# Performance work log

Hardware: AMD Instinct MI355X
Metric: run time of the kernel (lower is better)

The kernel has to match this reference:

```python
import jax, jax.numpy as jnp
import numpy as np

# ---- static configuration (matches init_kwargs / input_specs) ----
B, DIM, H, W = 2, 32, 512, 512
FOLD, P, HDIM, NCLS, CV = 8, 2, 96, 16, 96
S = P * P                      # superpixels per tile
h, w = H // FOLD, W // FOLD    # 64, 64 tile size
N = h * w                      # pixels per tile

# ---- static SSN neighbor tables (init label map -> 9 candidate spixels) ----
_lab = np.repeat(np.repeat(np.arange(S).reshape(P, P), h // P, 0), w // P, 1).reshape(-1)
_sy, _sx = _lab // P, _lab % P
_dy = np.repeat(np.array([-1, 0, 1]), 3)[:, None]
_dx = np.tile(np.array([-1, 0, 1]), 3)[:, None]
_ny, _nx = _sy[None] + _dy, _sx[None] + _dx
_valid = (_ny >= 0) & (_ny < P) & (_nx >= 0) & (_nx < P)
NBR = jnp.asarray(np.where(_valid, _ny * P + _nx, 0), dtype=jnp.int32)  # [9,N]
VALID = jnp.asarray(_valid)                                             # [9,N]

def _conv1x1(x, Wk, bk):
    return jnp.einsum('oc,bchw->bohw', Wk, x) + bk[None, :, None, None]

def _tiles(t):  # 'b c (f1 h) (f2 w) -> (b f1 f2) c h w'
    Bq, C = t.shape[:2]
    return t.reshape(Bq, C, FOLD, h, FOLD, w).transpose(0, 2, 4, 1, 3, 5).reshape(Bq * FOLD * FOLD, C, h, w)

def _pool(t):  # adaptive avg pool (h,w)->(P,P); returns [b,C,S]
    b, C = t.shape[:2]
    return t.reshape(b, C, P, h // P, P, w // P).mean((3, 5)).reshape(b, C, S)

def _affinity(Fp, cen):
    # Fp [b,Ctot,N], cen [b,Ctot,S]; squared-euclid dist pixel->9 neighbor spixels,
    # sparse softmax over the 9 candidates, then scatter to dense [b,S,N] affinity.
    d = (Fp * Fp).sum(1)[:, None, :] + (cen * cen).sum(1)[:, :, None] \
        - 2.0 * jnp.einsum('bcn,bcs->bsn', Fp, cen)          # [b,S,N]
    b = Fp.shape[0]
    idx = jnp.broadcast_to(NBR[None], (b, 9, N))
    d9 = jnp.where(VALID[None], jnp.take_along_axis(d, idx, axis=1), 1e16)
    aff = jax.nn.softmax(-d9, axis=1)                        # [b,9,N]
    bi = jnp.arange(b)[:, None, None]
    ni = jnp.arange(N)[None, None, :]
    return jnp.zeros((b, S, N), Fp.dtype).at[bi, idx, ni].add(jnp.where(VALID[None], aff, 0.0))

def setup_inputs():
    k = jax.random.split(jax.random.key(0), 6)
    return {
        'x': jax.random.normal(k[0], (B, DIM, H, W), jnp.float32),
        'feat': jax.random.normal(k[1], (B, CV, H, W), jnp.float32),
        'sdf_data': jax.random.normal(k[2], (B, DIM - 1, H, W), jnp.float32),
        'Wf': 0.1 * jax.random.normal(k[3], (HDIM, DIM), jnp.float32),
        'bf': jnp.zeros((HDIM,), jnp.float32),
        'Wsdf': 0.1 * jax.random.normal(k[4], (HDIM, DIM - 1), jnp.float32),
        'bsdf': jnp.zeros((HDIM,), jnp.float32),
        'gt': jax.random.randint(k[5], (B, H, W), 0, NCLS, jnp.int32),
    }

def _cluster(x, feat, sdf_data, Wf, bf, Wsdf, bsdf):
    hsi = _conv1x1(x, Wf, bf)
    sdf = _conv1x1(sdf_data, Wsdf, bsdf)
    pf = _tiles(feat).reshape(-1, CV, N)      # per-tile pixel (value) features
    df = _tiles(hsi).reshape(-1, HDIM, N)     # deep features
    sf = _tiles(sdf).reshape(-1, HDIM, N)     # sdf features
    b = pf.shape[0]
    cen_pf = _pool(pf.reshape(b, CV, h, w))
    cen_df = _pool(df.reshape(b, HDIM, h, w))
    cen_sf = _pool(sf.reshape(b, HDIM, h, w))
    value_centers = cen_pf.transpose(0, 2, 1)                # [b,S,C]
    Fall = jnp.concatenate([pf, df, sf], 1)
    # SSN iter 0: soft affinity, update pixel-feature centroids
    A0 = _affinity(Fall, jnp.concatenate([cen_pf, cen_df, cen_sf], 1))
    cen_pf = jnp.einsum('bsn,bcn->bcs', A0, pf) / (A0.sum(-1)[:, None, :] + 1e-16)
    # SSN iter 1 (last): final dense affinity; torch computes this under no_grad
    sim = jax.lax.stop_gradient(_affinity(Fall, jnp.concatenate([cen_pf, cen_df, cen_sf], 1)))
    mask = jax.nn.one_hot(jnp.argmax(sim, 1), S, axis=1, dtype=sim.dtype)   # hard argmax mask [b,S,N]
    sim = sim * mask
    out = (jnp.einsum('bsn,bnc->bsc', sim, pf.transpose(0, 2, 1)) + value_centers) \
          / (sim.sum(-1, keepdims=True) + 1.0)
    center_feat = out.reshape(B, FOLD * FOLD * S, CV)
    mask5 = mask.reshape(B, FOLD * FOLD, S, h, w)
    return center_feat, mask5

def _gen_labels(gt, mask5):
    T = FOLD * FOLD
    coef = jnp.arange(S, dtype=mask5.dtype).reshape(1, 1, S, 1, 1)
    small = (mask5 * coef).sum(2) + jnp.arange(0, T * S, S, dtype=mask5.dtype).reshape(1, T, 1, 1)
    spix_map = small.reshape(B, FOLD, FOLD, h, w).transpose(0, 1, 3, 2, 4).reshape(B, H, W)
    gt_r = gt.reshape(B, FOLD, h, FOLD, w).transpose(0, 1, 3, 2, 4).reshape(B, T, h, w) + 1
    gt_filt = (gt_r[:, :, None].astype(mask5.dtype) * mask5).reshape(B, T, S, N).astype(jnp.int32)
    count = jax.nn.one_hot(gt_filt, NCLS + 1, dtype=jnp.float32).sum(3)   # [B,T,S,NCLS+1]
    labels = count[..., 1:].transpose(0, 3, 1, 2).reshape(B, NCLS, T * S)
    return labels, spix_map

def reference(x, feat, sdf_data, Wf, bf, Wsdf, bsdf, gt):
    center_feat, mask5 = _cluster(x, feat, sdf_data, Wf, bf, Wsdf, bsdf)
    labels, spix_map = _gen_labels(gt, jax.lax.stop_gradient(mask5))
    return center_feat, labels, spix_map
```

## Files before the change

kernel.cpp:

```cpp
#include <hip/hip_runtime.h>
#include <hip/hip_bf16.h>


#define OFF_POOLX   0
#define OFF_POOLS   16384
#define OFF_CENPF0  32256
#define OFF_UDF     81408
#define OFF_USF     97792
#define OFF_GCONST  113664
#define OFF_NORM0   114176
#define OFF_NUM1    114688
#define OFF_DEN1    163840
#define OFF_CENPF1  164352
#define OFF_NORM1   213504
#define OFF_OUTNUM  214016
#define OFF_OUTDEN  263168
#define OFF_LABELS  263680
#define OFF_G       271872

#define OUT_CF 0
#define OUT_LB 49152
#define OUT_SP 57344

typedef float f32x4 __attribute__((ext_vector_type(4)));
typedef short bf16x8 __attribute__((ext_vector_type(8)));

__device__ __forceinline__ float bf2f(unsigned short u) {
  return __uint_as_float(((unsigned)u) << 16);
}
__device__ __forceinline__ unsigned short f2bf(float f) {
  return (unsigned short)(__float_as_uint(f) >> 16);
}

__global__ __launch_bounds__(256) void k_pool(const float* __restrict__ x,
    const float* __restrict__ feat, const float* __restrict__ sdf,
    float* __restrict__ ws) {
  int plane = blockIdx.x, f1 = blockIdx.y, tid = threadIdx.x;
  int b = plane / 159, ch = plane % 159;
  const float* src; int c, C, cls;
  if (ch < 32)      { src = x;    C = 32; c = ch;      cls = 0; }
  else if (ch < 63) { src = sdf;  C = 31; c = ch - 32; cls = 1; }
  else              { src = feat; C = 96; c = ch - 63; cls = 2; }
  const float* base = src + ((size_t)(b*C + c)*512 + f1*64)*512;
  int half = tid >> 7, col4 = tid & 127;
  const float* p0 = base + (size_t)half*512 + (size_t)col4*4;
  float4 v[16];
  float acc0 = 0.f, acc1 = 0.f;
  #pragma unroll
  for (int i = 0; i < 16; ++i)
    v[i] = *reinterpret_cast<const float4*>(p0 + (size_t)i*1024);
  #pragma unroll
  for (int i = 0; i < 16; ++i) { float4 t = v[i]; acc0 += t.x + t.y + t.z + t.w; }
  #pragma unroll
  for (int i = 0; i < 16; ++i)
    v[i] = *reinterpret_cast<const float4*>(p0 + (size_t)(16 + i)*1024);
  #pragma unroll
  for (int i = 0; i < 16; ++i) { float4 t = v[i]; acc1 += t.x + t.y + t.z + t.w; }
  acc0 += __shfl_xor(acc0, 1, 64); acc0 += __shfl_xor(acc0, 2, 64); acc0 += __shfl_xor(acc0, 4, 64);
  acc1 += __shfl_xor(acc1, 1, 64); acc1 += __shfl_xor(acc1, 2, 64); acc1 += __shfl_xor(acc1, 4, 64);
  __shared__ float part[32][2];
  int lane = tid & 63;
  if ((lane & 7) == 0) {
    int f2 = col4 >> 4, qx = (col4 >> 3) & 1;
    part[(f2*2 + qx)*2 + 0][half] = acc0;
    part[(f2*2 + qx)*2 + 1][half] = acc1;
  }
  __syncthreads();
  if (tid < 32) {
    float v2 = (part[tid][0] + part[tid][1]) * (1.f/1024.f);
    int f2 = tid >> 2, qx = (tid >> 1) & 1, qy = tid & 1;
    int tile = b*64 + f1*8 + f2, s = qy*2 + qx;
    float* dst;
    if (cls == 0)      dst = ws + OFF_POOLX  + (tile*32 + c)*4;
    else if (cls == 1) dst = ws + OFF_POOLS  + (tile*31 + c)*4;
    else               dst = ws + OFF_CENPF0 + (tile*96 + c)*4;
    dst[s] = v2;
  }
}

__global__ __launch_bounds__(384) void k_centers(const float* __restrict__ Wf,
    const float* __restrict__ bfv, const float* __restrict__ Wsdf,
    const float* __restrict__ bsdf, float* __restrict__ ws) {
  int tile = blockIdx.x, tid = threadIdx.x;
  __shared__ float px[128];
  __shared__ float ps[124];
  __shared__ float cdf[384];
  __shared__ float csf[384];
  __shared__ float redg[4], redn[4];
  if (tid < 128) px[tid] = ws[OFF_POOLX + tile*128 + tid];
  if (tid < 124) ps[tid] = ws[OFF_POOLS + tile*124 + tid];
  if (tid < 4) { redg[tid] = 0.f; redn[tid] = 0.f; }
  __syncthreads();
  int c = tid % 96, s = tid / 96;
  float bc = bfv[c];
  float a = bc;
  for (int k = 0; k < 32; ++k) a += Wf[c*32 + k] * px[k*4 + s];
  cdf[c*4 + s] = a;
  float bs = bsdf[c];
  float a2 = bs;
  for (int k = 0; k < 31; ++k) a2 += Wsdf[c*31 + k] * ps[k*4 + s];
  csf[c*4 + s] = a2;
  atomicAdd(&redg[s], 2.f*(bc*a + bs*a2) - (a*a + a2*a2));
  float cp = ws[OFF_CENPF0 + tile*384 + c*4 + s];
  atomicAdd(&redn[s], cp*cp);
  __syncthreads();
  if (tid < 128) {
    int s2 = tid >> 5, k = tid & 31;
    float u = 0.f;
    for (int c2 = 0; c2 < 96; ++c2) u += Wf[c2*32 + k] * cdf[c2*4 + s2];
    ws[OFF_UDF + tile*128 + tid] = u;
  } else if (tid < 252) {
    int t2 = tid - 128, s2 = t2 / 31, k = t2 % 31;
    float u = 0.f;
    for (int c2 = 0; c2 < 96; ++c2) u += Wsdf[c2*31 + k] * csf[c2*4 + s2];
    ws[OFF_USF + tile*124 + t2] = u;
  }
  if (tid < 4) { ws[OFF_GCONST + tile*4 + tid] = redg[tid]; ws[OFF_NORM0 + tile*4 + tid] = redn[tid]; }
}

__global__ __launch_bounds__(256) void k_pass2(const float* __restrict__ x,
    const float* __restrict__ feat, const float* __restrict__ sdf,
    float* __restrict__ ws) {
  int wg = blockIdx.x, tile = wg >> 2, seg = wg & 3, tid = threadIdx.x;
  int b = tile >> 6, tl = tile & 63, f1 = tl >> 3, f2 = tl & 7;
  __shared__ float s_cpf0[384];
  __shared__ float s_udf[128];
  __shared__ float s_usf[124];
  __shared__ float s_gc[4], s_n0[4];
  __shared__ __align__(16) unsigned short s_pfT[96][264];
  __shared__ __align__(16) unsigned short s_aT[16][264];
  for (int i = tid; i < 384; i += 256) s_cpf0[i] = ws[OFF_CENPF0 + tile*384 + i];
  if (tid < 128) s_udf[tid] = ws[OFF_UDF + tile*128 + tid];
  if (tid < 124) s_usf[tid] = ws[OFF_USF + tile*124 + tid];
  if (tid < 4) { s_gc[tid] = ws[OFF_GCONST + tile*4 + tid]; s_n0[tid] = ws[OFF_NORM0 + tile*4 + tid]; }
  for (int i = tid; i < 16*264; i += 256) (&s_aT[0][0])[i] = 0;
  __syncthreads();
  int lane = tid & 63, wave = tid >> 6;
  int mrow = lane & 15, quad = lane >> 4;
  f32x4 zero4 = {0.f, 0.f, 0.f, 0.f};
  f32x4 accC[6] = {zero4, zero4, zero4, zero4, zero4, zero4};
  float dden[4] = {0.f, 0.f, 0.f, 0.f};
  for (int chunk = 0; chunk < 4; ++chunk) {
    int p = seg*1024 + chunk*256 + tid;
    int y = p >> 6, xx = p & 63;
    int go = (f1*64 + y)*512 + f2*64 + xx;
    const float* xp = x   + (size_t)b*32*262144 + go;
    const float* sp = sdf + (size_t)b*31*262144 + go;
    const float* fp = feat+ (size_t)b*96*262144 + go;
    float vv[16];
    float d0=0.f,d1=0.f,d2=0.f,d3=0.f;
    #pragma unroll
    for (int kb = 0; kb < 32; kb += 16) {
      #pragma unroll
      for (int j = 0; j < 16; ++j) vv[j] = xp[(size_t)(kb + j)*262144];
      #pragma unroll
      for (int j = 0; j < 16; ++j) {
        float v = vv[j]; int k = kb + j;
        d0 += v*s_udf[k]; d1 += v*s_udf[32+k]; d2 += v*s_udf[64+k]; d3 += v*s_udf[96+k];
      }
    }
    {
      #pragma unroll
      for (int j = 0; j < 16; ++j) vv[j] = sp[(size_t)j*262144];
      #pragma unroll
      for (int j = 0; j < 16; ++j) {
        float v = vv[j];
        d0 += v*s_usf[j]; d1 += v*s_usf[31+j]; d2 += v*s_usf[62+j]; d3 += v*s_usf[93+j];
      }
      #pragma unroll
      for (int j = 0; j < 15; ++j) vv[j] = sp[(size_t)(16 + j)*262144];
      #pragma unroll
      for (int j = 0; j < 15; ++j) {
        float v = vv[j]; int k = 16 + j;
        d0 += v*s_usf[k]; d1 += v*s_usf[31+k]; d2 += v*s_usf[62+k]; d3 += v*s_usf[93+k];
      }
    }
    float g0 = 2.f*d0 + s_gc[0], g1 = 2.f*d1 + s_gc[1];
    float g2 = 2.f*d2 + s_gc[2], g3 = 2.f*d3 + s_gc[3];
    int gbase = OFF_G + (tile << 14) + p;
    ws[gbase] = g0; ws[gbase + 4096] = g1; ws[gbase + 8192] = g2; ws[gbase + 12288] = g3;
    float p0=0.f,p1=0.f,p2=0.f,p3=0.f;
    #pragma unroll
    for (int cb = 0; cb < 96; cb += 16) {
      #pragma unroll
      for (int j = 0; j < 16; ++j) vv[j] = fp[(size_t)(cb + j)*262144];
      #pragma unroll
      for (int j = 0; j < 16; ++j) {
        float v = vv[j]; int cc = cb + j;
        s_pfT[cc][tid] = f2bf(v);
        p0 += v*s_cpf0[cc*4+0]; p1 += v*s_cpf0[cc*4+1]; p2 += v*s_cpf0[cc*4+2]; p3 += v*s_cpf0[cc*4+3];
      }
    }
    float sc0 = g0 + 2.f*p0 - s_n0[0];
    float sc1 = g1 + 2.f*p1 - s_n0[1];
    float sc2 = g2 + 2.f*p2 - s_n0[2];
    float sc3 = g3 + 2.f*p3 - s_n0[3];
    float m = fmaxf(fmaxf(sc0, sc1), fmaxf(sc2, sc3));
    float e0 = expf(sc0 - m), e1 = expf(sc1 - m), e2 = expf(sc2 - m), e3 = expf(sc3 - m);
    float inv = 1.f / (e0 + e1 + e2 + e3);
    float a0 = e0*inv, a1 = e1*inv, a2 = e2*inv, a3 = e3*inv;
    s_aT[0][tid] = f2bf(a0); s_aT[1][tid] = f2bf(a1);
    s_aT[2][tid] = f2bf(a2); s_aT[3][tid] = f2bf(a3);
    dden[0] += a0; dden[1] += a1; dden[2] += a2; dden[3] += a3;
    __syncthreads();
    #pragma unroll
    for (int kk = 0; kk < 2; ++kk) {
      int k0 = (wave*2 + kk)*32 + quad*8;
      bf16x8 bfrag = *reinterpret_cast<const bf16x8*>(&s_aT[mrow][k0]);
      #pragma unroll
      for (int mt = 0; mt < 6; ++mt) {
        bf16x8 afrag = *reinterpret_cast<const bf16x8*>(&s_pfT[mt*16 + mrow][k0]);
        accC[mt] = __builtin_amdgcn_mfma_f32_16x16x32_bf16(afrag, bfrag, accC[mt], 0, 0, 0);
      }
    }
    __syncthreads();
  }
  if (mrow < 4) {
    #pragma unroll
    for (int mt = 0; mt < 6; ++mt)
      #pragma unroll
      for (int r = 0; r < 4; ++r) {
        int c = mt*16 + quad*4 + r;
        atomicAdd(&ws[OFF_NUM1 + (tile*96 + c)*4 + mrow], accC[mt][r]);
      }
  }
  for (int m2 = 1; m2 < 64; m2 <<= 1) {
    dden[0] += __shfl_xor(dden[0], m2, 64); dden[1] += __shfl_xor(dden[1], m2, 64);
    dden[2] += __shfl_xor(dden[2], m2, 64); dden[3] += __shfl_xor(dden[3], m2, 64);
  }
  if (lane == 0) {
    atomicAdd(&ws[OFF_DEN1 + tile*4 + 0], dden[0]);
    atomicAdd(&ws[OFF_DEN1 + tile*4 + 1], dden[1]);
    atomicAdd(&ws[OFF_DEN1 + tile*4 + 2], dden[2]);
    atomicAdd(&ws[OFF_DEN1 + tile*4 + 3], dden[3]);
  }
}

__global__ __launch_bounds__(384) void k_fin1(float* __restrict__ ws) {
  int tile = blockIdx.x, tid = threadIdx.x;
  __shared__ float red[4];
  if (tid < 4) red[tid] = 0.f;
  __syncthreads();
  int c = tid % 96, s = tid / 96;
  float den = ws[OFF_DEN1 + tile*4 + s];
  float v = ws[OFF_NUM1 + (tile*96 + c)*4 + s] / (den + 1e-16f);
  ws[OFF_CENPF1 + (tile*96 + c)*4 + s] = v;
  atomicAdd(&red[s], v*v);
  __syncthreads();
  if (tid < 4) ws[OFF_NORM1 + tile*4 + tid] = red[tid];
}

__global__ __launch_bounds__(256) void k_pass3(const float* __restrict__ feat,
    const int* __restrict__ gt, float* __restrict__ ws, float* __restrict__ out) {
  int wg = blockIdx.x, tile = wg >> 2, seg = wg & 3, tid = threadIdx.x;
  int b = tile >> 6, tl = tile & 63, f1 = tl >> 3, f2 = tl & 7;
  __shared__ float s_cpf1[384];
  __shared__ float s_n1[4];
  __shared__ __align__(16) unsigned short s_pfT[96][264];
  __shared__ __align__(16) unsigned short s_aT[16][264];
  __shared__ float s_hist[64];
  for (int i = tid; i < 384; i += 256) s_cpf1[i] = ws[OFF_CENPF1 + tile*384 + i];
  if (tid < 4) s_n1[tid] = ws[OFF_NORM1 + tile*4 + tid];
  if (tid < 64) s_hist[tid] = 0.f;
  for (int i = tid; i < 16*264; i += 256) (&s_aT[0][0])[i] = 0;
  __syncthreads();
  int lane = tid & 63, wave = tid >> 6;
  int mrow = lane & 15, quad = lane >> 4;
  f32x4 zero4 = {0.f, 0.f, 0.f, 0.f};
  f32x4 accC[6] = {zero4, zero4, zero4, zero4, zero4, zero4};
  float oden[4] = {0.f, 0.f, 0.f, 0.f};
  for (int chunk = 0; chunk < 4; ++chunk) {
    int p = seg*1024 + chunk*256 + tid;
    int y = p >> 6, xx = p & 63;
    int go = (f1*64 + y)*512 + f2*64 + xx;
    int gbase = OFF_G + (tile << 14) + p;
    float g0 = ws[gbase], g1 = ws[gbase + 4096], g2 = ws[gbase + 8192], g3 = ws[gbase + 12288];
    const float* fp = feat + (size_t)b*96*262144 + go;
    float vv[16];
    float p0=0.f,p1=0.f,p2=0.f,p3=0.f;
    #pragma unroll
    for (int cb = 0; cb < 96; cb += 16) {
      #pragma unroll
      for (int j = 0; j < 16; ++j) vv[j] = fp[(size_t)(cb + j)*262144];
      #pragma unroll
      for (int j = 0; j < 16; ++j) {
        float v = vv[j]; int cc = cb + j;
        s_pfT[cc][tid] = f2bf(v);
        p0 += v*s_cpf1[cc*4+0]; p1 += v*s_cpf1[cc*4+1]; p2 += v*s_cpf1[cc*4+2]; p3 += v*s_cpf1[cc*4+3];
      }
    }
    float sc0 = g0 + 2.f*p0 - s_n1[0];
    float sc1 = g1 + 2.f*p1 - s_n1[1];
    float sc2 = g2 + 2.f*p2 - s_n1[2];
    float sc3 = g3 + 2.f*p3 - s_n1[3];
    int ss = 0; float best = sc0;
    if (sc1 > best) { best = sc1; ss = 1; }
    if (sc2 > best) { best = sc2; ss = 2; }
    if (sc3 > best) { best = sc3; ss = 3; }
    float se = expf(sc0-best) + expf(sc1-best) + expf(sc2-best) + expf(sc3-best);
    float sim = 1.f / se;
    unsigned short sb = f2bf(sim);
    s_aT[0][tid] = (ss == 0) ? sb : (unsigned short)0;
    s_aT[1][tid] = (ss == 1) ? sb : (unsigned short)0;
    s_aT[2][tid] = (ss == 2) ? sb : (unsigned short)0;
    s_aT[3][tid] = (ss == 3) ? sb : (unsigned short)0;
    oden[ss] += sim;
    int gv = gt[b*262144 + go];
    atomicAdd(&s_hist[ss*16 + gv], 1.f);
    out[OUT_SP + b*262144 + go] = (float)(tl*4 + ss);
    __syncthreads();
    #pragma unroll
    for (int kk = 0; kk < 2; ++kk) {
      int k0 = (wave*2 + kk)*32 + quad*8;
      bf16x8 bfrag = *reinterpret_cast<const bf16x8*>(&s_aT[mrow][k0]);
      #pragma unroll
      for (int mt = 0; mt < 6; ++mt) {
        bf16x8 afrag = *reinterpret_cast<const bf16x8*>(&s_pfT[mt*16 + mrow][k0]);
        accC[mt] = __builtin_amdgcn_mfma_f32_16x16x32_bf16(afrag, bfrag, accC[mt], 0, 0, 0);
      }
    }
    __syncthreads();
  }
  if (mrow < 4) {
    #pragma unroll
    for (int mt = 0; mt < 6; ++mt)
      #pragma unroll
      for (int r = 0; r < 4; ++r) {
        int c = mt*16 + quad*4 + r;
        atomicAdd(&ws[OFF_OUTNUM + (tile*96 + c)*4 + mrow], accC[mt][r]);
      }
  }
  for (int m2 = 1; m2 < 64; m2 <<= 1) {
    oden[0] += __shfl_xor(oden[0], m2, 64); oden[1] += __shfl_xor(oden[1], m2, 64);
    oden[2] += __shfl_xor(oden[2], m2, 64); oden[3] += __shfl_xor(oden[3], m2, 64);
  }
  if (lane == 0) {
    atomicAdd(&ws[OFF_OUTDEN + tile*4 + 0], oden[0]);
    atomicAdd(&ws[OFF_OUTDEN + tile*4 + 1], oden[1]);
    atomicAdd(&ws[OFF_OUTDEN + tile*4 + 2], oden[2]);
    atomicAdd(&ws[OFF_OUTDEN + tile*4 + 3], oden[3]);
  }
  if (tid < 64) atomicAdd(&ws[OFF_LABELS + tile*64 + tid], s_hist[tid]);
}

__global__ __launch_bounds__(384) void k_out(const float* __restrict__ ws,
                                             float* __restrict__ out) {
  int tile = blockIdx.x, tid = threadIdx.x;
  int b = tile >> 6, tl = tile & 63;
  int c = tid % 96, s = tid / 96;
  float od = ws[OFF_OUTDEN + tile*4 + s];
  float v = (ws[OFF_OUTNUM + (tile*96 + c)*4 + s] + ws[OFF_CENPF0 + (tile*96 + c)*4 + s]) / (od + 1.f);
  out[OUT_CF + (size_t)(b*256 + tl*4 + s)*96 + c] = v;
  if (tid < 64) {
    int s2 = tid >> 4, cls = tid & 15;
    float cnt = ws[OFF_LABELS + tile*64 + tid];
    out[OUT_LB + (b*16 + cls)*256 + tl*4 + s2] = cnt;
  }
}

extern "C" void kernel_launch(void* const* d_in, const int* in_sizes, int n_in,
                              void* d_out, int out_size, void* d_ws, size_t ws_size,
                              hipStream_t stream) {
  const float* x    = (const float*)d_in[0];
  const float* feat = (const float*)d_in[1];
  const float* sdf  = (const float*)d_in[2];
  const float* Wf   = (const float*)d_in[3];
  const float* bfv  = (const float*)d_in[4];
  const float* Wsdf = (const float*)d_in[5];
  const float* bsdf = (const float*)d_in[6];
  const int* gt = (const int*)d_in[7];
  float* ws = (float*)d_ws;
  float* out = (float*)d_out;

  hipMemsetAsync(ws + OFF_NUM1, 0,
                 (size_t)(OFF_LABELS + 128*64 - OFF_NUM1) * sizeof(float), stream);

  k_pool   <<<dim3(318, 8), 256, 0, stream>>>(x, feat, sdf, ws);
  k_centers<<<128, 384, 0, stream>>>(Wf, bfv, Wsdf, bsdf, ws);
  k_pass2  <<<512, 256, 0, stream>>>(x, feat, sdf, ws);
  k_fin1   <<<128, 384, 0, stream>>>(ws);
  k_pass3  <<<512, 256, 0, stream>>>(feat, gt, ws, out);
  k_out    <<<128, 384, 0, stream>>>(ws, out);
}
```

Measured before the change: 507.8 us.

## Stash pooled inputs in tile-contiguous layout during pooling pass for later passes

The pooling kernel now also writes every input value it reads into a workspace stash arranged per tile, per 256-pixel group and per channel. The later passes then read from this stash instead of doing strided gathers over the NCHW inputs. The intermediate G values are also stored interleaved as one float4 per pixel, so each is a single vector store and load. This turns the later passes' reads into contiguous per-channel rows, at the cost of an extra full write and re-read of about 159 channels of data through the workspace.

```diff
diff --git a/kernel.cpp b/kernel.cpp
--- a/kernel.cpp
+++ b/kernel.cpp
@@ -17,6 +17,9 @@
 #define OFF_OUTDEN  263168
 #define OFF_LABELS  263680
 #define OFF_G       271872
+#define OFF_STASH   16777216
+#define CHSTRIDE    256
+#define GSTRIDE     40704
 
 #define OUT_CF 0
 #define OUT_LB 49152
@@ -41,40 +44,51 @@
   if (ch < 32)      { src = x;    C = 32; c = ch;      cls = 0; }
   else if (ch < 63) { src = sdf;  C = 31; c = ch - 32; cls = 1; }
   else              { src = feat; C = 96; c = ch - 63; cls = 2; }
-  const float* base = src + ((size_t)(b*C + c)*512 + f1*64)*512;
-  int half = tid >> 7, col4 = tid & 127;
-  const float* p0 = base + (size_t)half*512 + (size_t)col4*4;
+  int wave = tid >> 6, L = tid & 63;
+  const float* base = src + ((size_t)(b*C + c)*512 + f1*64 + wave*16)*512 + L*4;
+  int tile0 = b*64 + f1*8;
+  int stash0 = OFF_STASH + ch*CHSTRIDE + (L & 15)*4;
+  float accE = 0.f, accO = 0.f;
   float4 v[16];
-  float acc0 = 0.f, acc1 = 0.f;
   #pragma unroll
-  for (int i = 0; i < 16; ++i)
-    v[i] = *reinterpret_cast<const float4*>(p0 + (size_t)i*1024);
-  #pragma unroll
-  for (int i = 0; i < 16; ++i) { float4 t = v[i]; acc0 += t.x + t.y + t.z + t.w; }
-  #pragma unroll
-  for (int i = 0; i < 16; ++i)
-    v[i] = *reinterpret_cast<const float4*>(p0 + (size_t)(16 + i)*1024);
-  #pragma unroll
-  for (int i = 0; i < 16; ++i) { float4 t = v[i]; acc1 += t.x + t.y + t.z + t.w; }
-  acc0 += __shfl_xor(acc0, 1, 64); acc0 += __shfl_xor(acc0, 2, 64); acc0 += __shfl_xor(acc0, 4, 64);
-  acc1 += __shfl_xor(acc1, 1, 64); acc1 += __shfl_xor(acc1, 2, 64); acc1 += __shfl_xor(acc1, 4, 64);
-  __shared__ float part[32][2];
-  int lane = tid & 63;
-  if ((lane & 7) == 0) {
-    int f2 = col4 >> 4, qx = (col4 >> 3) & 1;
-    part[(f2*2 + qx)*2 + 0][half] = acc0;
-    part[(f2*2 + qx)*2 + 1][half] = acc1;
+  for (int jb = 0; jb < 2; ++jb) {
+    #pragma unroll
+    for (int j = 0; j < 16; ++j)
+      v[j] = *reinterpret_cast<const float4*>(base + (size_t)(jb*16 + j)*256);
+    #pragma unroll
+    for (int j = 0; j < 16; ++j) {
+      int jj = jb*16 + j;
+      int row = wave*16 + (jj >> 1);
+      int colHalf = jj & 1;
+      int f2 = colHalf*4 + (L >> 4);
+      int g = row >> 2;
+      int px = (row & 3)*64;
+      float4 t = v[j];
+      *reinterpret_cast<float4*>(ws + stash0 +
+          (size_t)((tile0 + f2)*16 + g)*GSTRIDE + px) = t;
+      float s4 = t.x + t.y + t.z + t.w;
+      if (colHalf == 0) accE += s4; else accO += s4;
+    }
+  }
+  accE += __shfl_xor(accE, 1, 64); accE += __shfl_xor(accE, 2, 64); accE += __shfl_xor(accE, 4, 64);
+  accO += __shfl_xor(accO, 1, 64); accO += __shfl_xor(accO, 2, 64); accO += __shfl_xor(accO, 4, 64);
+  __shared__ float part[4][16];
+  if ((L & 7) == 0) {
+    int qx = (L >> 3) & 1, fE = L >> 4;
+    part[wave][fE*2 + qx] = accE;
+    part[wave][(4 + fE)*2 + qx] = accO;
   }
   __syncthreads();
   if (tid < 32) {
-    float v2 = (part[tid][0] + part[tid][1]) * (1.f/1024.f);
     int f2 = tid >> 2, qx = (tid >> 1) & 1, qy = tid & 1;
-    int tile = b*64 + f1*8 + f2, s = qy*2 + qx;
+    int idx = f2*2 + qx;
+    float val = (part[qy*2][idx] + part[qy*2 + 1][idx]) * (1.f/1024.f);
+    int tile = tile0 + f2, s = qy*2 + qx;
     float* dst;
     if (cls == 0)      dst = ws + OFF_POOLX  + (tile*32 + c)*4;
     else if (cls == 1) dst = ws + OFF_POOLS  + (tile*31 + c)*4;
     else               dst = ws + OFF_CENPF0 + (tile*96 + c)*4;
-    dst[s] = v2;
+    dst[s] = val;
   }
 }
 
@@ -122,7 +136,6 @@
     const float* __restrict__ feat, const float* __restrict__ sdf,
     float* __restrict__ ws) {
   int wg = blockIdx.x, tile = wg >> 2, seg = wg & 3, tid = threadIdx.x;
-  int b = tile >> 6, tl = tile & 63, f1 = tl >> 3, f2 = tl & 7;
   __shared__ float s_cpf0[384];
   __shared__ float s_udf[128];
   __shared__ float s_usf[124];
@@ -141,18 +154,15 @@
   f32x4 accC[6] = {zero4, zero4, zero4, zero4, zero4, zero4};
   float dden[4] = {0.f, 0.f, 0.f, 0.f};
   for (int chunk = 0; chunk < 4; ++chunk) {
+    int g = seg*4 + chunk;
     int p = seg*1024 + chunk*256 + tid;
-    int y = p >> 6, xx = p & 63;
-    int go = (f1*64 + y)*512 + f2*64 + xx;
-    const float* xp = x   + (size_t)b*32*262144 + go;
-    const float* sp = sdf + (size_t)b*31*262144 + go;
-    const float* fp = feat+ (size_t)b*96*262144 + go;
+    const float* SB = ws + OFF_STASH + (size_t)(tile*16 + g)*GSTRIDE + tid;
     float vv[16];
     float d0=0.f,d1=0.f,d2=0.f,d3=0.f;
     #pragma unroll
     for (int kb = 0; kb < 32; kb += 16) {
       #pragma unroll
-      for (int j = 0; j < 16; ++j) vv[j] = xp[(size_t)(kb + j)*262144];
+      for (int j = 0; j < 16; ++j) vv[j] = SB[(size_t)(kb + j)*CHSTRIDE];
       #pragma unroll
       for (int j = 0; j < 16; ++j) {
         float v = vv[j]; int k = kb + j;
@@ -161,14 +171,14 @@
     }
     {
       #pragma unroll
-      for (int j = 0; j < 16; ++j) vv[j] = sp[(size_t)j*262144];
+      for (int j = 0; j < 16; ++j) vv[j] = SB[(size_t)(32 + j)*CHSTRIDE];
       #pragma unroll
       for (int j = 0; j < 16; ++j) {
         float v = vv[j];
         d0 += v*s_usf[j]; d1 += v*s_usf[31+j]; d2 += v*s_usf[62+j]; d3 += v*s_usf[93+j];
       }
       #pragma unroll
-      for (int j = 0; j < 15; ++j) vv[j] = sp[(size_t)(16 + j)*262144];
+      for (int j = 0; j < 15; ++j) vv[j] = SB[(size_t)(48 + j)*CHSTRIDE];
       #pragma unroll
       for (int j = 0; j < 15; ++j) {
         float v = vv[j]; int k = 16 + j;
@@ -177,13 +187,15 @@
     }
     float g0 = 2.f*d0 + s_gc[0], g1 = 2.f*d1 + s_gc[1];
     float g2 = 2.f*d2 + s_gc[2], g3 = 2.f*d3 + s_gc[3];
-    int gbase = OFF_G + (tile << 14) + p;
-    ws[gbase] = g0; ws[gbase + 4096] = g1; ws[gbase + 8192] = g2; ws[gbase + 12288] = g3;
+    {
+      f32x4 gv = {g0, g1, g2, g3};
+      *reinterpret_cast<f32x4*>(ws + OFF_G + ((size_t)tile << 14) + (size_t)p*4) = gv;
+    }
     float p0=0.f,p1=0.f,p2=0.f,p3=0.f;
     #pragma unroll
     for (int cb = 0; cb < 96; cb += 16) {
       #pragma unroll
-      for (int j = 0; j < 16; ++j) vv[j] = fp[(size_t)(cb + j)*262144];
+      for (int j = 0; j < 16; ++j) vv[j] = SB[(size_t)(63 + cb + j)*CHSTRIDE];
       #pragma unroll
       for (int j = 0; j < 16; ++j) {
         float v = vv[j]; int cc = cb + j;
@@ -270,18 +282,18 @@
   f32x4 accC[6] = {zero4, zero4, zero4, zero4, zero4, zero4};
   float oden[4] = {0.f, 0.f, 0.f, 0.f};
   for (int chunk = 0; chunk < 4; ++chunk) {
+    int g = seg*4 + chunk;
     int p = seg*1024 + chunk*256 + tid;
     int y = p >> 6, xx = p & 63;
     int go = (f1*64 + y)*512 + f2*64 + xx;
-    int gbase = OFF_G + (tile << 14) + p;
-    float g0 = ws[gbase], g1 = ws[gbase + 4096], g2 = ws[gbase + 8192], g3 = ws[gbase + 12288];
-    const float* fp = feat + (size_t)b*96*262144 + go;
+    f32x4 gv = *reinterpret_cast<const f32x4*>(ws + OFF_G + ((size_t)tile << 14) + (size_t)p*4);
+    const float* SB = ws + OFF_STASH + (size_t)(tile*16 + g)*GSTRIDE + tid;
     float vv[16];
     float p0=0.f,p1=0.f,p2=0.f,p3=0.f;
     #pragma unroll
     for (int cb = 0; cb < 96; cb += 16) {
       #pragma unroll
-      for (int j = 0; j < 16; ++j) vv[j] = fp[(size_t)(cb + j)*262144];
+      for (int j = 0; j < 16; ++j) vv[j] = SB[(size_t)(63 + cb + j)*CHSTRIDE];
       #pragma unroll
       for (int j = 0; j < 16; ++j) {
         float v = vv[j]; int cc = cb + j;
@@ -289,10 +301,10 @@
         p0 += v*s_cpf1[cc*4+0]; p1 += v*s_cpf1[cc*4+1]; p2 += v*s_cpf1[cc*4+2]; p3 += v*s_cpf1[cc*4+3];
       }
     }
-    float sc0 = g0 + 2.f*p0 - s_n1[0];
-    float sc1 = g1 + 2.f*p1 - s_n1[1];
-    float sc2 = g2 + 2.f*p2 - s_n1[2];
-    float sc3 = g3 + 2.f*p3 - s_n1[3];
+    float sc0 = gv[0] + 2.f*p0 - s_n1[0];
+    float sc1 = gv[1] + 2.f*p1 - s_n1[1];
+    float sc2 = gv[2] + 2.f*p2 - s_n1[2];
+    float sc3 = gv[3] + 2.f*p3 - s_n1[3];
     int ss = 0; float best = sc0;
     if (sc1 > best) { best = sc1; ss = 1; }
     if (sc2 > best) { best = sc2; ss = 2; }
@@ -305,8 +317,8 @@
     s_aT[2][tid] = (ss == 2) ? sb : (unsigned short)0;
     s_aT[3][tid] = (ss == 3) ? sb : (unsigned short)0;
     oden[ss] += sim;
-    int gv = gt[b*262144 + go];
-    atomicAdd(&s_hist[ss*16 + gv], 1.f);
+    int gv2 = gt[b*262144 + go];
+    atomicAdd(&s_hist[ss*16 + gv2], 1.f);
     out[OUT_SP + b*262144 + go] = (float)(tl*4 + ss);
     __syncthreads();
     #pragma unroll
```

New measurement: 561.6 us. +10.6%, slower.

## Vectorize pass loads across waves, fold memset and fin1 into other kernels

Applied to the files above, without the earlier changes.

In pass2 and pass3, each thread now loads float4 over four adjacent pixels, and the channel reduction is split across waves. Partial sums are combined through shared memory, which adds two barriers per chunk. The G buffer layout becomes pixel-interleaved so it can be written and read as one float4. The workspace memset is folded into k_pool, and the k_fin1 normalization is folded into the pass3 prologue, removing two launches.

```diff
diff --git a/kernel.cpp b/kernel.cpp
--- a/kernel.cpp
+++ b/kernel.cpp
@@ -17,6 +17,8 @@
 #define OFF_OUTDEN  263168
 #define OFF_LABELS  263680
 #define OFF_G       271872
+#define ZERO_BASE   OFF_NUM1
+#define ZERO_LEN    157184
 
 #define OUT_CF 0
 #define OUT_LB 49152
@@ -24,6 +26,7 @@
 
 typedef float f32x4 __attribute__((ext_vector_type(4)));
 typedef short bf16x8 __attribute__((ext_vector_type(8)));
+typedef unsigned short u16x4 __attribute__((ext_vector_type(4)));
 
 __device__ __forceinline__ float bf2f(unsigned short u) {
   return __uint_as_float(((unsigned)u) << 16);
@@ -36,6 +39,13 @@
     const float* __restrict__ feat, const float* __restrict__ sdf,
     float* __restrict__ ws) {
   int plane = blockIdx.x, f1 = blockIdx.y, tid = threadIdx.x;
+  {
+    int lb = blockIdx.y * gridDim.x + blockIdx.x;
+    if (tid < 64) {
+      int zi = lb * 64 + tid;
+      if (zi < ZERO_LEN) ws[ZERO_BASE + zi] = 0.f;
+    }
+  }
   int b = plane / 159, ch = plane % 159;
   const float* src; int c, C, cls;
   if (ch < 32)      { src = x;    C = 32; c = ch;      cls = 0; }
@@ -44,18 +54,18 @@
   const float* base = src + ((size_t)(b*C + c)*512 + f1*64)*512;
   int half = tid >> 7, col4 = tid & 127;
   const float* p0 = base + (size_t)half*512 + (size_t)col4*4;
-  float4 v[16];
+  f32x4 v[16];
   float acc0 = 0.f, acc1 = 0.f;
   #pragma unroll
   for (int i = 0; i < 16; ++i)
-    v[i] = *reinterpret_cast<const float4*>(p0 + (size_t)i*1024);
+    v[i] = *reinterpret_cast<const f32x4*>(p0 + (size_t)i*1024);
   #pragma unroll
-  for (int i = 0; i < 16; ++i) { float4 t = v[i]; acc0 += t.x + t.y + t.z + t.w; }
+  for (int i = 0; i < 16; ++i) { f32x4 t = v[i]; acc0 += t[0] + t[1] + t[2] + t[3]; }
   #pragma unroll
   for (int i = 0; i < 16; ++i)
-    v[i] = *reinterpret_cast<const float4*>(p0 + (size_t)(16 + i)*1024);
+    v[i] = *reinterpret_cast<const f32x4*>(p0 + (size_t)(16 + i)*1024);
   #pragma unroll
-  for (int i = 0; i < 16; ++i) { float4 t = v[i]; acc1 += t.x + t.y + t.z + t.w; }
+  for (int i = 0; i < 16; ++i) { f32x4 t = v[i]; acc1 += t[0] + t[1] + t[2] + t[3]; }
   acc0 += __shfl_xor(acc0, 1, 64); acc0 += __shfl_xor(acc0, 2, 64); acc0 += __shfl_xor(acc0, 4, 64);
   acc1 += __shfl_xor(acc1, 1, 64); acc1 += __shfl_xor(acc1, 2, 64); acc1 += __shfl_xor(acc1, 4, 64);
   __shared__ float part[32][2];
@@ -129,6 +139,7 @@
   __shared__ float s_gc[4], s_n0[4];
   __shared__ __align__(16) unsigned short s_pfT[96][264];
   __shared__ __align__(16) unsigned short s_aT[16][264];
+  __shared__ __align__(16) float s_part[2][8][260];
   for (int i = tid; i < 384; i += 256) s_cpf0[i] = ws[OFF_CENPF0 + tile*384 + i];
   if (tid < 128) s_udf[tid] = ws[OFF_UDF + tile*128 + tid];
   if (tid < 124) s_usf[tid] = ws[OFF_USF + tile*124 + tid];
@@ -137,59 +148,88 @@
   __syncthreads();
   int lane = tid & 63, wave = tid >> 6;
   int mrow = lane & 15, quad = lane >> 4;
+  int q4 = lane * 4;
   f32x4 zero4 = {0.f, 0.f, 0.f, 0.f};
   f32x4 accC[6] = {zero4, zero4, zero4, zero4, zero4, zero4};
   float dden[4] = {0.f, 0.f, 0.f, 0.f};
   for (int chunk = 0; chunk < 4; ++chunk) {
-    int p = seg*1024 + chunk*256 + tid;
-    int y = p >> 6, xx = p & 63;
-    int go = (f1*64 + y)*512 + f2*64 + xx;
-    const float* xp = x   + (size_t)b*32*262144 + go;
-    const float* sp = sdf + (size_t)b*31*262144 + go;
-    const float* fp = feat+ (size_t)b*96*262144 + go;
-    float vv[16];
-    float d0=0.f,d1=0.f,d2=0.f,d3=0.f;
-    #pragma unroll
-    for (int kb = 0; kb < 32; kb += 16) {
-      #pragma unroll
-      for (int j = 0; j < 16; ++j) vv[j] = xp[(size_t)(kb + j)*262144];
-      #pragma unroll
-      for (int j = 0; j < 16; ++j) {
-        float v = vv[j]; int k = kb + j;
-        d0 += v*s_udf[k]; d1 += v*s_udf[32+k]; d2 += v*s_udf[64+k]; d3 += v*s_udf[96+k];
-      }
-    }
-    {
-      #pragma unroll
-      for (int j = 0; j < 16; ++j) vv[j] = sp[(size_t)j*262144];
-      #pragma unroll
-      for (int j = 0; j < 16; ++j) {
-        float v = vv[j];
-        d0 += v*s_usf[j]; d1 += v*s_usf[31+j]; d2 += v*s_usf[62+j]; d3 += v*s_usf[93+j];
-      }
-      #pragma unroll
-      for (int j = 0; j < 15; ++j) vv[j] = sp[(size_t)(16 + j)*262144];
-      #pragma unroll
-      for (int j = 0; j < 15; ++j) {
-        float v = vv[j]; int k = 16 + j;
-        d0 += v*s_usf[k]; d1 += v*s_usf[31+k]; d2 += v*s_usf[62+k]; d3 += v*s_usf[93+k];
-      }
-    }
+    int pq = seg*1024 + chunk*256 + q4;
+    int goq = (f1*64 + (pq >> 6))*512 + f2*64 + (pq & 63);
+    const float* xq = x   + (size_t)(b*32)*262144 + goq;
+    const float* sq = sdf + (size_t)(b*31)*262144 + goq;
+    const float* fq = feat+ (size_t)(b*96)*262144 + goq;
+    f32x4 dpd[4] = {zero4, zero4, zero4, zero4};
+    f32x4 dpp[4] = {zero4, zero4, zero4, zero4};
+    f32x4 vv[8];
+    #pragma unroll
+    for (int i = 0; i < 8; ++i)
+      vv[i] = *reinterpret_cast<const f32x4*>(xq + (size_t)(wave + 4*i)*262144);
+    #pragma unroll
+    for (int i = 0; i < 8; ++i) {
+      int ch = wave + 4*i;
+      #pragma unroll
+      for (int s = 0; s < 4; ++s) dpd[s] += vv[i] * s_udf[s*32 + ch];
+    }
+    #pragma unroll
+    for (int i = 0; i < 8; ++i)
+      if (wave + 4*i < 31)
+        vv[i] = *reinterpret_cast<const f32x4*>(sq + (size_t)(wave + 4*i)*262144);
+    #pragma unroll
+    for (int i = 0; i < 8; ++i) {
+      int ch = wave + 4*i;
+      if (ch < 31) {
+        #pragma unroll
+        for (int s = 0; s < 4; ++s) dpd[s] += vv[i] * s_usf[s*31 + ch];
+      }
+    }
+    #pragma unroll
+    for (int r = 0; r < 3; ++r) {
+      #pragma unroll
+      for (int i = 0; i < 8; ++i)
+        vv[i] = *reinterpret_cast<const f32x4*>(fq + (size_t)(wave + 4*(r*8 + i))*262144);
+      #pragma unroll
+      for (int i = 0; i < 8; ++i) {
+        int ch = wave + 4*(r*8 + i);
+        u16x4 uu = { f2bf(vv[i][0]), f2bf(vv[i][1]), f2bf(vv[i][2]), f2bf(vv[i][3]) };
+        *reinterpret_cast<u16x4*>(&s_pfT[ch][q4]) = uu;
+        #pragma unroll
+        for (int s = 0; s < 4; ++s) dpp[s] += vv[i] * s_cpf0[ch*4 + s];
+      }
+    }
+    if (wave >= 2) {
+      #pragma unroll
+      for (int s = 0; s < 4; ++s) {
+        *reinterpret_cast<f32x4*>(&s_part[wave-2][s][q4]) = dpd[s];
+        *reinterpret_cast<f32x4*>(&s_part[wave-2][4+s][q4]) = dpp[s];
+      }
+    }
+    __syncthreads();
+    if (wave < 2) {
+      #pragma unroll
+      for (int s = 0; s < 4; ++s) {
+        f32x4 t = *reinterpret_cast<f32x4*>(&s_part[wave][s][q4]);
+        t += dpd[s];
+        *reinterpret_cast<f32x4*>(&s_part[wave][s][q4]) = t;
+        f32x4 t2 = *reinterpret_cast<f32x4*>(&s_part[wave][4+s][q4]);
+        t2 += dpp[s];
+        *reinterpret_cast<f32x4*>(&s_part[wave][4+s][q4]) = t2;
+      }
+    }
+    __syncthreads();
+    float d0 = s_part[0][0][tid] + s_part[1][0][tid];
+    float d1 = s_part[0][1][tid] + s_part[1][1][tid];
+    float d2 = s_part[0][2][tid] + s_part[1][2][tid];
+    float d3 = s_part[0][3][tid] + s_part[1][3][tid];
+    float p0 = s_part[0][4][tid] + s_part[1][4][tid];
+    float p1 = s_part[0][5][tid] + s_part[1][5][tid];
+    float p2 = s_part[0][6][tid] + s_part[1][6][tid];
+    float p3 = s_part[0][7][tid] + s_part[1][7][tid];
     float g0 = 2.f*d0 + s_gc[0], g1 = 2.f*d1 + s_gc[1];
     float g2 = 2.f*d2 + s_gc[2], g3 = 2.f*d3 + s_gc[3];
-    int gbase = OFF_G + (tile << 14) + p;
-    ws[gbase] = g0; ws[gbase + 4096] = g1; ws[gbase + 8192] = g2; ws[gbase + 12288] = g3;
-    float p0=0.f,p1=0.f,p2=0.f,p3=0.f;
-    #pragma unroll
-    for (int cb = 0; cb < 96; cb += 16) {
-      #pragma unroll
-      for (int j = 0; j < 16; ++j) vv[j] = fp[(size_t)(cb + j)*262144];
-      #pragma unroll
-      for (int j = 0; j < 16; ++j) {
-        float v = vv[j]; int cc = cb + j;
-        s_pfT[cc][tid] = f2bf(v);
-        p0 += v*s_cpf0[cc*4+0]; p1 += v*s_cpf0[cc*4+1]; p2 += v*s_cpf0[cc*4+2]; p3 += v*s_cpf0[cc*4+3];
-      }
+    int p = seg*1024 + chunk*256 + tid;
+    {
+      f32x4 gv = {g0, g1, g2, g3};
+      *reinterpret_cast<f32x4*>(ws + OFF_G + ((size_t)tile << 14) + (size_t)p*4) = gv;
     }
     float sc0 = g0 + 2.f*p0 - s_n0[0];
     float sc1 = g1 + 2.f*p1 - s_n0[1];
@@ -236,20 +276,6 @@
   }
 }
 
-__global__ __launch_bounds__(384) void k_fin1(float* __restrict__ ws) {
-  int tile = blockIdx.x, tid = threadIdx.x;
-  __shared__ float red[4];
-  if (tid < 4) red[tid] = 0.f;
-  __syncthreads();
-  int c = tid % 96, s = tid / 96;
-  float den = ws[OFF_DEN1 + tile*4 + s];
-  float v = ws[OFF_NUM1 + (tile*96 + c)*4 + s] / (den + 1e-16f);
-  ws[OFF_CENPF1 + (tile*96 + c)*4 + s] = v;
-  atomicAdd(&red[s], v*v);
-  __syncthreads();
-  if (tid < 4) ws[OFF_NORM1 + tile*4 + tid] = red[tid];
-}
-
 __global__ __launch_bounds__(256) void k_pass3(const float* __restrict__ feat,
     const int* __restrict__ gt, float* __restrict__ ws, float* __restrict__ out) {
   int wg = blockIdx.x, tile = wg >> 2, seg = wg & 3, tid = threadIdx.x;
@@ -258,41 +284,72 @@
   __shared__ float s_n1[4];
   __shared__ __align__(16) unsigned short s_pfT[96][264];
   __shared__ __align__(16) unsigned short s_aT[16][264];
+  __shared__ __align__(16) float s_part[2][4][260];
   __shared__ float s_hist[64];
-  for (int i = tid; i < 384; i += 256) s_cpf1[i] = ws[OFF_CENPF1 + tile*384 + i];
-  if (tid < 4) s_n1[tid] = ws[OFF_NORM1 + tile*4 + tid];
+  if (tid < 4) s_n1[tid] = 0.f;
   if (tid < 64) s_hist[tid] = 0.f;
   for (int i = tid; i < 16*264; i += 256) (&s_aT[0][0])[i] = 0;
   __syncthreads();
+  for (int i = tid; i < 384; i += 256) {
+    float den = ws[OFF_DEN1 + tile*4 + (i & 3)];
+    float v = ws[OFF_NUM1 + tile*384 + i] / (den + 1e-16f);
+    s_cpf1[i] = v;
+    atomicAdd(&s_n1[i & 3], v*v);
+  }
+  __syncthreads();
   int lane = tid & 63, wave = tid >> 6;
   int mrow = lane & 15, quad = lane >> 4;
+  int q4 = lane * 4;
   f32x4 zero4 = {0.f, 0.f, 0.f, 0.f};
   f32x4 accC[6] = {zero4, zero4, zero4, zero4, zero4, zero4};
   float oden[4] = {0.f, 0.f, 0.f, 0.f};
   for (int chunk = 0; chunk < 4; ++chunk) {
+    int pq = seg*1024 + chunk*256 + q4;
+    int goq = (f1*64 + (pq >> 6))*512 + f2*64 + (pq & 63);
+    const float* fq = feat + (size_t)(b*96)*262144 + goq;
+    f32x4 dpp[4] = {zero4, zero4, zero4, zero4};
+    f32x4 vv[8];
+    #pragma unroll
+    for (int r = 0; r < 3; ++r) {
+      #pragma unroll
+      for (int i = 0; i < 8; ++i)
+        vv[i] = *reinterpret_cast<const f32x4*>(fq + (size_t)(wave + 4*(r*8 + i))*262144);
+      #pragma unroll
+      for (int i = 0; i < 8; ++i) {
+        int ch = wave + 4*(r*8 + i);
+        u16x4 uu = { f2bf(vv[i][0]), f2bf(vv[i][1]), f2bf(vv[i][2]), f2bf(vv[i][3]) };
+        *reinterpret_cast<u16x4*>(&s_pfT[ch][q4]) = uu;
+        #pragma unroll
+        for (int s = 0; s < 4; ++s) dpp[s] += vv[i] * s_cpf1[ch*4 + s];
+      }
+    }
+    if (wave >= 2) {
+      #pragma unroll
+      for (int s = 0; s < 4; ++s)
+        *reinterpret_cast<f32x4*>(&s_part[wave-2][s][q4]) = dpp[s];
+    }
+    __syncthreads();
+    if (wave < 2) {
+      #pragma unroll
+      for (int s = 0; s < 4; ++s) {
+        f32x4 t = *reinterpret_cast<f32x4*>(&s_part[wave][s][q4]);
+        t += dpp[s];
+        *reinterpret_cast<f32x4*>(&s_part[wave][s][q4]) = t;
+      }
+    }
+    __syncthreads();
     int p = seg*1024 + chunk*256 + tid;
     int y = p >> 6, xx = p & 63;
     int go = (f1*64 + y)*512 + f2*64 + xx;
-    int gbase = OFF_G + (tile << 14) + p;
-    float g0 = ws[gbase], g1 = ws[gbase + 4096], g2 = ws[gbase + 8192], g3 = ws[gbase + 12288];
-    const float* fp = feat + (size_t)b*96*262144 + go;
-    float vv[16];
-    float p0=0.f,p1=0.f,p2=0.f,p3=0.f;
-    #pragma unroll
-    for (int cb = 0; cb < 96; cb += 16) {
-      #pragma unroll
-      for (int j = 0; j < 16; ++j) vv[j] = fp[(size_t)(cb + j)*262144];
-      #pragma unroll
-      for (int j = 0; j < 16; ++j) {
-        float v = vv[j]; int cc = cb + j;
-        s_pfT[cc][tid] = f2bf(v);
-        p0 += v*s_cpf1[cc*4+0]; p1 += v*s_cpf1[cc*4+1]; p2 += v*s_cpf1[cc*4+2]; p3 += v*s_cpf1[cc*4+3];
-      }
-    }
-    float sc0 = g0 + 2.f*p0 - s_n1[0];
-    float sc1 = g1 + 2.f*p1 - s_n1[1];
-    float sc2 = g2 + 2.f*p2 - s_n1[2];
-    float sc3 = g3 + 2.f*p3 - s_n1[3];
+    f32x4 gv = *reinterpret_cast<const f32x4*>(ws + OFF_G + ((size_t)tile << 14) + (size_t)p*4);
+    float p0 = s_part[0][0][tid] + s_part[1][0][tid];
+    float p1 = s_part[0][1][tid] + s_part[1][1][tid];
+    float p2 = s_part[0][2][tid] + s_part[1][2][tid];
+    float p3 = s_part[0][3][tid] + s_part[1][3][tid];
+    float sc0 = gv[0] + 2.f*p0 - s_n1[0];
+    float sc1 = gv[1] + 2.f*p1 - s_n1[1];
+    float sc2 = gv[2] + 2.f*p2 - s_n1[2];
+    float sc3 = gv[3] + 2.f*p3 - s_n1[3];
     int ss = 0; float best = sc0;
     if (sc1 > best) { best = sc1; ss = 1; }
     if (sc2 > best) { best = sc2; ss = 2; }
@@ -305,8 +362,8 @@
     s_aT[2][tid] = (ss == 2) ? sb : (unsigned short)0;
     s_aT[3][tid] = (ss == 3) ? sb : (unsigned short)0;
     oden[ss] += sim;
-    int gv = gt[b*262144 + go];
-    atomicAdd(&s_hist[ss*16 + gv], 1.f);
+    int gvv = gt[b*262144 + go];
+    atomicAdd(&s_hist[ss*16 + gvv], 1.f);
     out[OUT_SP + b*262144 + go] = (float)(tl*4 + ss);
     __syncthreads();
     #pragma unroll
@@ -372,13 +429,9 @@
   float* ws = (float*)d_ws;
   float* out = (float*)d_out;
 
-  hipMemsetAsync(ws + OFF_NUM1, 0,
-                 (size_t)(OFF_LABELS + 128*64 - OFF_NUM1) * sizeof(float), stream);
-
   k_pool   <<<dim3(318, 8), 256, 0, stream>>>(x, feat, sdf, ws);
   k_centers<<<128, 384, 0, stream>>>(Wf, bfv, Wsdf, bsdf, ws);
   k_pass2  <<<512, 256, 0, stream>>>(x, feat, sdf, ws);
-  k_fin1   <<<128, 384, 0, stream>>>(ws);
   k_pass3  <<<512, 256, 0, stream>>>(feat, gt, ws, out);
   k_out    <<<128, 384, 0, stream>>>(ws, out);
 }
```

Result: faster. 491.8 us (-3.2%).
